# Performance work log

Hardware: AMD Instinct MI355X
Metric: run time of the kernel (lower is better)

Reference implementation:

```python
import jax, jax.numpy as jnp
import numpy as np

D_MODEL = 256
NUM_HEAD = 4
D_HEAD = D_MODEL // NUM_HEAD
B, N, M = 1, 512, 512


def setup_inputs() -> dict:
    key = jax.random.key(0)
    ks = jax.random.split(key, 13)
    s = 1.0 / np.sqrt(D_MODEL)
    inp = {
        'input_q': jax.random.normal(ks[0], (B, N, D_MODEL), jnp.float32),
        'input_k': jax.random.normal(ks[1], (B, M, D_MODEL), jnp.float32),
        'input_v': jax.random.normal(ks[2], (B, M, D_MODEL), jnp.float32),
        'input_p': jax.random.normal(ks[3], (B, N, M, D_MODEL), jnp.float32),
        'key_masks': jnp.zeros((B, M), dtype=bool),
        'Wq': jax.random.normal(ks[4], (D_MODEL, D_MODEL), jnp.float32) * s,
        'bq': jnp.zeros((D_MODEL,), jnp.float32),
        'Wk': jax.random.normal(ks[5], (D_MODEL, D_MODEL), jnp.float32) * s,
        'bk': jnp.zeros((D_MODEL,), jnp.float32),
        'Wv': jax.random.normal(ks[6], (D_MODEL, D_MODEL), jnp.float32) * s,
        'bv': jnp.zeros((D_MODEL,), jnp.float32),
        'Wp': jax.random.normal(ks[7], (D_MODEL, D_MODEL), jnp.float32) * s,
        'bp': jnp.zeros((D_MODEL,), jnp.float32),
    }
    return inp


def reference(input_q, input_k, input_v, input_p, key_masks,
              Wq, bq, Wk, bk, Wv, bv, Wp, bp):
    H, Dh = NUM_HEAD, D_HEAD
    b, n, _ = input_q.shape
    m = input_k.shape[1]
    # linear projections (PyTorch Linear: x @ W.T + b)
    q = (input_q @ Wq.T + bq).reshape(b, n, H, Dh).transpose(0, 2, 1, 3)   # (B,H,N,Dh)
    k = (input_k @ Wk.T + bk).reshape(b, m, H, Dh).transpose(0, 2, 1, 3)   # (B,H,M,Dh)
    v = (input_v @ Wv.T + bv).reshape(b, m, H, Dh).transpose(0, 2, 1, 3)   # (B,H,M,Dh)
    p = (input_p @ Wp.T + bp).reshape(b, n, m, H, Dh)                      # (B,N,M,H,Dh)
    # content scores + per-pair RPE scores (q dot p)
    scores = (jnp.einsum('bhnd,bhmd->bhnm', q, k)
              + jnp.einsum('bhnd,bnmhd->bhnm', q, p)) / np.sqrt(Dh)
    scores = jnp.where(key_masks[:, None, None, :], -jnp.inf, scores)
    attn = jax.nn.softmax(scores, axis=-1)                                 # (B,H,N,M)
    hidden = jnp.einsum('bhnm,bhmd->bhnd', attn, v)
    hidden = hidden.transpose(0, 2, 1, 3).reshape(b, n, H * Dh)            # (B,N,C)
    return hidden
```

## Files before the change

kernel.cpp:

```cpp
#include <hip/hip_runtime.h>
#include <math.h>

#define DMODEL 256
#define NSEQ   512
#define MSEQ   512
#define NHEAD  4
#define DHEAD  64

#define WS_Q      0
#define WS_K      131072
#define WS_V      262144
#define WS_WPE    393216
#define WS_SCORES 917504

__global__ __launch_bounds__(256) void proj_qkv(
    const float* __restrict__ xq, const float* __restrict__ xk,
    const float* __restrict__ xv,
    const float* __restrict__ Wq, const float* __restrict__ bq,
    const float* __restrict__ Wk, const float* __restrict__ bk,
    const float* __restrict__ Wv, const float* __restrict__ bv,
    float* __restrict__ ws)
{
    int bid = blockIdx.x;
    int mat = bid >> 6;
    int rb  = bid & 63;
    const float* X; const float* W; const float* b; float* Y;
    if (mat == 0)      { X = xq; W = Wq; b = bq; Y = ws + WS_Q; }
    else if (mat == 1) { X = xk; W = Wk; b = bk; Y = ws + WS_K; }
    else               { X = xv; W = Wv; b = bv; Y = ws + WS_V; }

    int c  = threadIdx.x;
    int r0 = rb * 8;
    float acc[8];
    float bias = b[c];
#pragma unroll
    for (int r = 0; r < 8; ++r) acc[r] = bias;

    const float4* Wrow = (const float4*)(W + (size_t)c * DMODEL);
    for (int d4 = 0; d4 < 64; ++d4) {
        float4 w = Wrow[d4];
#pragma unroll
        for (int r = 0; r < 8; ++r) {
            float4 x = ((const float4*)(X + (size_t)(r0 + r) * DMODEL))[d4];
            acc[r] += w.x * x.x + w.y * x.y + w.z * x.z + w.w * x.w;
        }
    }
#pragma unroll
    for (int r = 0; r < 8; ++r)
        Y[(size_t)(r0 + r) * DMODEL + c] = acc[r];
}

__global__ __launch_bounds__(256) void make_wpeff(
    const float* __restrict__ Wp, float* __restrict__ ws)
{
    const float* q   = ws + WS_Q;
    float*       wpe = ws + WS_WPE;
    int n0 = blockIdx.x * 2;
    int d  = threadIdx.x;

    const float* q0 = q + (size_t)n0 * DMODEL;
    const float* q1 = q0 + DMODEL;

    float acc0[4] = {0.f, 0.f, 0.f, 0.f};
    float acc1[4] = {0.f, 0.f, 0.f, 0.f};
#pragma unroll
    for (int h = 0; h < 4; ++h) {
        for (int dh = 0; dh < 64; ++dh) {
            int c = h * 64 + dh;
            float w = Wp[(size_t)c * DMODEL + d];
            acc0[h] += q0[c] * w;
            acc1[h] += q1[c] * w;
        }
    }
    *(float4*)&wpe[(size_t)n0 * 1024 + d * 4] =
        make_float4(acc0[0], acc0[1], acc0[2], acc0[3]);
    *(float4*)&wpe[(size_t)(n0 + 1) * 1024 + d * 4] =
        make_float4(acc1[0], acc1[1], acc1[2], acc1[3]);
}

__global__ __launch_bounds__(256) void p_scores(
    const float* __restrict__ Xp, float* __restrict__ ws)
{
    const float* wpe    = ws + WS_WPE;
    float*       scores = ws + WS_SCORES;

    int bid  = blockIdx.x;
    int n    = bid >> 1;
    int m0   = (bid & 1) * 256;
    int tid  = threadIdx.x;
    int wv   = tid >> 6;
    int lane = tid & 63;
    int p    = lane & 15;
    int r3   = lane >> 4;

    const float4* wp4 = (const float4*)(wpe + (size_t)n * 1024);
    float4 w[4][4];
#pragma unroll
    for (int j = 0; j < 4; ++j)
#pragma unroll
        for (int c = 0; c < 4; ++c)
            w[j][c] = wp4[4 * p + 64 * j + c];

    __shared__ float sm[4][256];

    const float4* base4 =
        (const float4*)Xp + ((size_t)n * MSEQ + m0 + wv * 64) * 64;

#pragma unroll 2
    for (int g = 0; g < 16; ++g) {
        int rbase = (g * 4 + r3) * 64 + p;
        float4 xv0 = base4[rbase + 0];
        float4 xv1 = base4[rbase + 16];
        float4 xv2 = base4[rbase + 32];
        float4 xv3 = base4[rbase + 48];

        float sh[4] = {0.f, 0.f, 0.f, 0.f};
        {
            const float4 xs[4] = {xv0, xv1, xv2, xv3};
#pragma unroll
            for (int j = 0; j < 4; ++j) {
                const float* xc = &xs[j].x;
#pragma unroll
                for (int c = 0; c < 4; ++c) {
                    const float* wf = &w[j][c].x;
#pragma unroll
                    for (int h = 0; h < 4; ++h)
                        sh[h] += xc[c] * wf[h];
                }
            }
        }
#pragma unroll
        for (int off = 1; off < 16; off <<= 1) {
#pragma unroll
            for (int h = 0; h < 4; ++h)
                sh[h] += __shfl_xor(sh[h], off);
        }
        if (p == 0) {
            int ml = wv * 64 + g * 4 + r3;
            sm[0][ml] = sh[0];
            sm[1][ml] = sh[1];
            sm[2][ml] = sh[2];
            sm[3][ml] = sh[3];
        }
    }
    __syncthreads();

    size_t ob = (size_t)n * MSEQ + m0 + tid;
    scores[0 * 262144 + ob] = sm[0][tid];
    scores[1 * 262144 + ob] = sm[1][tid];
    scores[2 * 262144 + ob] = sm[2][tid];
    scores[3 * 262144 + ob] = sm[3][tid];
}

__global__ __launch_bounds__(256) void qk_scores(
    const float* __restrict__ bp, float* __restrict__ ws)
{
    const float* q      = ws + WS_Q;
    const float* k      = ws + WS_K;
    float*       scores = ws + WS_SCORES;

    int bid = blockIdx.x;
    int h   = bid >> 6;
    int nt  = (bid >> 3) & 7;
    int mt  = bid & 7;
    int n0  = nt * 64, m0 = mt * 64;

    __shared__ float qs[64][76];
    __shared__ float ks[64][76];
    __shared__ float qb[64];

    int tid = threadIdx.x;
#pragma unroll
    for (int rep = 0; rep < 4; ++rep) {
        int idx = rep * 1024 + tid * 4;
        int row = idx >> 6, col = idx & 63;
        *(float4*)&qs[row][col] =
            *(const float4*)&q[(size_t)(n0 + row) * DMODEL + h * 64 + col];
        *(float4*)&ks[row][col] =
            *(const float4*)&k[(size_t)(m0 + row) * DMODEL + h * 64 + col];
    }
    __syncthreads();

    if (tid < 64) {
        float s = 0.f;
        for (int dh = 0; dh < 64; ++dh) s += qs[tid][dh] * bp[h * 64 + dh];
        qb[tid] = s;
    }
    __syncthreads();

    int tn = tid >> 4, tm = tid & 15;
    float acc[4][4] = {};
    for (int kk = 0; kk < 64; kk += 4) {
        float4 qf[4], kf[4];
#pragma unroll
        for (int i = 0; i < 4; ++i) {
            qf[i] = *(const float4*)&qs[tn * 4 + i][kk];
            kf[i] = *(const float4*)&ks[tm * 4 + i][kk];
        }
#pragma unroll
        for (int i = 0; i < 4; ++i)
#pragma unroll
            for (int j = 0; j < 4; ++j)
                acc[i][j] += qf[i].x * kf[j].x + qf[i].y * kf[j].y +
                             qf[i].z * kf[j].z + qf[i].w * kf[j].w;
    }

#pragma unroll
    for (int i = 0; i < 4; ++i) {
        int n = n0 + tn * 4 + i;
        float qbn = qb[tn * 4 + i];
        float4* pp = (float4*)&scores[(size_t)h * 262144 +
                                      (size_t)n * MSEQ + m0 + tm * 4];
        float4 sp = *pp;
        sp.x = 0.125f * (sp.x + acc[i][0] + qbn);
        sp.y = 0.125f * (sp.y + acc[i][1] + qbn);
        sp.z = 0.125f * (sp.z + acc[i][2] + qbn);
        sp.w = 0.125f * (sp.w + acc[i][3] + qbn);
        *pp = sp;
    }
}

__global__ __launch_bounds__(256) void softmax_av(
    const unsigned char* __restrict__ mask,
    float* __restrict__ out, float* __restrict__ ws)
{
    const float* v      = ws + WS_V;
    const float* scores = ws + WS_SCORES;

    int bid = blockIdx.x;
    int h   = bid >> 6;
    int g   = bid & 63;
    int n0  = g * 8;

    __shared__ float  pl[MSEQ * 9];
    __shared__ float4 red4[256];
    __shared__ float  wred[4];

    int tid  = threadIdx.x;
    int lane = tid & 63, wv = tid >> 6;

    for (int j = 0; j < 8; ++j) {
        int n = n0 + j;
        const float* srow = scores + (size_t)h * 262144 + (size_t)n * MSEQ;
        float s0 = srow[tid];
        float s1 = srow[tid + 256];
        if (mask[tid])       s0 = -INFINITY;
        if (mask[tid + 256]) s1 = -INFINITY;

        float mx = fmaxf(s0, s1);
#pragma unroll
        for (int off = 32; off; off >>= 1) mx = fmaxf(mx, __shfl_xor(mx, off));
        if (lane == 0) wred[wv] = mx;
        __syncthreads();
        mx = fmaxf(fmaxf(wred[0], wred[1]), fmaxf(wred[2], wred[3]));

        float e0 = __expf(s0 - mx);
        float e1 = __expf(s1 - mx);
        float sm = e0 + e1;
#pragma unroll
        for (int off = 32; off; off >>= 1) sm += __shfl_xor(sm, off);
        __syncthreads();
        if (lane == 0) wred[wv] = sm;
        __syncthreads();
        sm = wred[0] + wred[1] + wred[2] + wred[3];
        float rinv = 1.0f / sm;

        pl[(size_t)tid * 9 + j]         = e0 * rinv;
        pl[(size_t)(tid + 256) * 9 + j] = e1 * rinv;
        __syncthreads();
    }

    int dhq = tid & 15, mq = tid >> 4;
    float acc[8][4] = {};
    for (int i = 0; i < 32; ++i) {
        int m = i * 16 + mq;
        float4 vv = *(const float4*)&v[(size_t)m * DMODEL + h * 64 + dhq * 4];
        float4 pa = *(const float4*)&pl[(size_t)m * 9];
        float4 pb = *(const float4*)&pl[(size_t)m * 9 + 4];
#pragma unroll
        for (int j = 0; j < 4; ++j) {
            float pv = (&pa.x)[j];
            acc[j][0] += pv * vv.x; acc[j][1] += pv * vv.y;
            acc[j][2] += pv * vv.z; acc[j][3] += pv * vv.w;
        }
#pragma unroll
        for (int j = 0; j < 4; ++j) {
            float pv = (&pb.x)[j];
            acc[4 + j][0] += pv * vv.x; acc[4 + j][1] += pv * vv.y;
            acc[4 + j][2] += pv * vv.z; acc[4 + j][3] += pv * vv.w;
        }
    }

    for (int j = 0; j < 8; ++j) {
        red4[mq * 16 + dhq] =
            make_float4(acc[j][0], acc[j][1], acc[j][2], acc[j][3]);
        __syncthreads();
        if (tid < 64) {
            int dq = tid >> 2, x = tid & 3;
            float s = 0.f;
#pragma unroll
            for (int qq = 0; qq < 16; ++qq)
                s += ((const float*)&red4[qq * 16 + dq])[x];
            out[(size_t)(n0 + j) * DMODEL + h * 64 + tid] = s;
        }
        __syncthreads();
    }
}

extern "C" void kernel_launch(void* const* d_in, const int* in_sizes, int n_in,
                              void* d_out, int out_size, void* d_ws,
                              size_t ws_size, hipStream_t stream)
{
    const float* xq = (const float*)d_in[0];
    const float* xk = (const float*)d_in[1];
    const float* xv = (const float*)d_in[2];
    const float* xp = (const float*)d_in[3];
    const unsigned char* mask = (const unsigned char*)d_in[4];
    const float* Wq = (const float*)d_in[5];
    const float* bq = (const float*)d_in[6];
    const float* Wk = (const float*)d_in[7];
    const float* bk = (const float*)d_in[8];
    const float* Wv = (const float*)d_in[9];
    const float* bv = (const float*)d_in[10];
    const float* Wp = (const float*)d_in[11];
    const float* bp = (const float*)d_in[12];
    float* out = (float*)d_out;
    float* ws  = (float*)d_ws;

    proj_qkv  <<<192,  256, 0, stream>>>(xq, xk, xv, Wq, bq, Wk, bk, Wv, bv, ws);
    make_wpeff<<<256,  256, 0, stream>>>(Wp, ws);
    p_scores  <<<1024, 256, 0, stream>>>(xp, ws);
    qk_scores <<<256,  256, 0, stream>>>(bp, ws);
    softmax_av<<<256,  256, 0, stream>>>(mask, out, ws);
}
```

Before: 108.1 us.

## Reorder QK before P-scores, use nontemporal loads for P, restructure helper kernels

The QK score kernel now runs before the P-score kernel and writes scaled QK scores, and the P-score kernel accumulates its scaled contribution into them. This replaces the old read-modify-write pass in QK and restructures QK as a per-row-group dot product over keys. The large input_p stream is read with nontemporal loads to avoid polluting the cache. make_wpeff now uses one block per row with q staged in shared memory, and softmax_av's probability layout is changed from stride 9 to stride 8 with a contiguous m ordering. The risk is more LDS bank conflicts from the stride-8 layout, and the P kernel now does a read-add-write on the score buffer.

```diff
diff --git a/kernel.cpp b/kernel.cpp
--- a/kernel.cpp
+++ b/kernel.cpp
@@ -4,14 +4,14 @@
 #define DMODEL 256
 #define NSEQ   512
 #define MSEQ   512
-#define NHEAD  4
-#define DHEAD  64
 
 #define WS_Q      0
 #define WS_K      131072
 #define WS_V      262144
 #define WS_WPE    393216
-#define WS_SCORES 917504
+#define WS_SQK    917504
+
+typedef float v4f __attribute__((ext_vector_type(4)));
 
 __global__ __launch_bounds__(256) void proj_qkv(
     const float* __restrict__ xq, const float* __restrict__ xk,
@@ -55,34 +55,85 @@
 {
     const float* q   = ws + WS_Q;
     float*       wpe = ws + WS_WPE;
-    int n0 = blockIdx.x * 2;
-    int d  = threadIdx.x;
-
-    const float* q0 = q + (size_t)n0 * DMODEL;
-    const float* q1 = q0 + DMODEL;
-
-    float acc0[4] = {0.f, 0.f, 0.f, 0.f};
-    float acc1[4] = {0.f, 0.f, 0.f, 0.f};
+    int n = blockIdx.x;
+    int d = threadIdx.x;
+
+    __shared__ float ql[256];
+    ql[d] = q[(size_t)n * DMODEL + d];
+    __syncthreads();
+
+    float acc[4];
 #pragma unroll
     for (int h = 0; h < 4; ++h) {
+        float a = 0.f;
+#pragma unroll 8
         for (int dh = 0; dh < 64; ++dh) {
             int c = h * 64 + dh;
-            float w = Wp[(size_t)c * DMODEL + d];
-            acc0[h] += q0[c] * w;
-            acc1[h] += q1[c] * w;
-        }
-    }
-    *(float4*)&wpe[(size_t)n0 * 1024 + d * 4] =
-        make_float4(acc0[0], acc0[1], acc0[2], acc0[3]);
-    *(float4*)&wpe[(size_t)(n0 + 1) * 1024 + d * 4] =
-        make_float4(acc1[0], acc1[1], acc1[2], acc1[3]);
+            a += ql[c] * Wp[(size_t)c * DMODEL + d];
+        }
+        acc[h] = a;
+    }
+    *(float4*)&wpe[(size_t)n * 1024 + d * 4] =
+        make_float4(acc[0], acc[1], acc[2], acc[3]);
+}
+
+__global__ __launch_bounds__(256) void qk_scores(
+    const float* __restrict__ bp, float* __restrict__ ws)
+{
+    const float* q   = ws + WS_Q;
+    const float* k   = ws + WS_K;
+    float*       sqk = ws + WS_SQK;
+
+    int bid = blockIdx.x;
+    int h   = bid >> 6;
+    int g   = bid & 63;
+    int n0  = g * 8;
+    int tid = threadIdx.x;
+
+    __shared__ float qls[8][64];
+    __shared__ float qb[8];
+
+    if (tid < 128) {
+        int row = tid >> 4, col = (tid & 15) * 4;
+        *(float4*)&qls[row][col] =
+            *(const float4*)&q[(size_t)(n0 + row) * DMODEL + h * 64 + col];
+    }
+    __syncthreads();
+    if (tid < 8) {
+        float s = 0.f;
+        for (int dh = 0; dh < 64; ++dh) s += qls[tid][dh] * bp[h * 64 + dh];
+        qb[tid] = s;
+    }
+    __syncthreads();
+
+    const float* ka = k + (size_t)tid * DMODEL + h * 64;
+    const float* kb = ka + (size_t)256 * DMODEL;
+    float acca[8] = {};
+    float accb[8] = {};
+#pragma unroll 4
+    for (int d4 = 0; d4 < 16; ++d4) {
+        float4 xa = *(const float4*)(ka + d4 * 4);
+        float4 xb = *(const float4*)(kb + d4 * 4);
+#pragma unroll
+        for (int j = 0; j < 8; ++j) {
+            float4 qq = *(const float4*)&qls[j][d4 * 4];
+            acca[j] += xa.x * qq.x + xa.y * qq.y + xa.z * qq.z + xa.w * qq.w;
+            accb[j] += xb.x * qq.x + xb.y * qq.y + xb.z * qq.z + xb.w * qq.w;
+        }
+    }
+#pragma unroll
+    for (int j = 0; j < 8; ++j) {
+        size_t base = (size_t)h * 262144 + (size_t)(n0 + j) * MSEQ;
+        sqk[base + tid]       = 0.125f * (acca[j] + qb[j]);
+        sqk[base + tid + 256] = 0.125f * (accb[j] + qb[j]);
+    }
 }
 
 __global__ __launch_bounds__(256) void p_scores(
     const float* __restrict__ Xp, float* __restrict__ ws)
 {
-    const float* wpe    = ws + WS_WPE;
-    float*       scores = ws + WS_SCORES;
+    const float* wpe = ws + WS_WPE;
+    float*       sqk = ws + WS_SQK;
 
     int bid  = blockIdx.x;
     int n    = bid >> 1;
@@ -103,29 +154,29 @@
 
     __shared__ float sm[4][256];
 
-    const float4* base4 =
-        (const float4*)Xp + ((size_t)n * MSEQ + m0 + wv * 64) * 64;
+    const v4f* base4 =
+        (const v4f*)Xp + ((size_t)n * MSEQ + m0 + wv * 64) * 64;
 
 #pragma unroll 2
     for (int g = 0; g < 16; ++g) {
         int rbase = (g * 4 + r3) * 64 + p;
-        float4 xv0 = base4[rbase + 0];
-        float4 xv1 = base4[rbase + 16];
-        float4 xv2 = base4[rbase + 32];
-        float4 xv3 = base4[rbase + 48];
+        v4f xv0 = __builtin_nontemporal_load(&base4[rbase + 0]);
+        v4f xv1 = __builtin_nontemporal_load(&base4[rbase + 16]);
+        v4f xv2 = __builtin_nontemporal_load(&base4[rbase + 32]);
+        v4f xv3 = __builtin_nontemporal_load(&base4[rbase + 48]);
 
         float sh[4] = {0.f, 0.f, 0.f, 0.f};
         {
-            const float4 xs[4] = {xv0, xv1, xv2, xv3};
+            const v4f xs[4] = {xv0, xv1, xv2, xv3};
 #pragma unroll
             for (int j = 0; j < 4; ++j) {
-                const float* xc = &xs[j].x;
 #pragma unroll
                 for (int c = 0; c < 4; ++c) {
+                    const float xc = xs[j][c];
                     const float* wf = &w[j][c].x;
 #pragma unroll
                     for (int h = 0; h < 4; ++h)
-                        sh[h] += xc[c] * wf[h];
+                        sh[h] += xc * wf[h];
                 }
             }
         }
@@ -146,78 +197,9 @@
     __syncthreads();
 
     size_t ob = (size_t)n * MSEQ + m0 + tid;
-    scores[0 * 262144 + ob] = sm[0][tid];
-    scores[1 * 262144 + ob] = sm[1][tid];
-    scores[2 * 262144 + ob] = sm[2][tid];
-    scores[3 * 262144 + ob] = sm[3][tid];
-}
-
-__global__ __launch_bounds__(256) void qk_scores(
-    const float* __restrict__ bp, float* __restrict__ ws)
-{
-    const float* q      = ws + WS_Q;
-    const float* k      = ws + WS_K;
-    float*       scores = ws + WS_SCORES;
-
-    int bid = blockIdx.x;
-    int h   = bid >> 6;
-    int nt  = (bid >> 3) & 7;
-    int mt  = bid & 7;
-    int n0  = nt * 64, m0 = mt * 64;
-
-    __shared__ float qs[64][76];
-    __shared__ float ks[64][76];
-    __shared__ float qb[64];
-
-    int tid = threadIdx.x;
-#pragma unroll
-    for (int rep = 0; rep < 4; ++rep) {
-        int idx = rep * 1024 + tid * 4;
-        int row = idx >> 6, col = idx & 63;
-        *(float4*)&qs[row][col] =
-            *(const float4*)&q[(size_t)(n0 + row) * DMODEL + h * 64 + col];
-        *(float4*)&ks[row][col] =
-            *(const float4*)&k[(size_t)(m0 + row) * DMODEL + h * 64 + col];
-    }
-    __syncthreads();
-
-    if (tid < 64) {
-        float s = 0.f;
-        for (int dh = 0; dh < 64; ++dh) s += qs[tid][dh] * bp[h * 64 + dh];
-        qb[tid] = s;
-    }
-    __syncthreads();
-
-    int tn = tid >> 4, tm = tid & 15;
-    float acc[4][4] = {};
-    for (int kk = 0; kk < 64; kk += 4) {
-        float4 qf[4], kf[4];
-#pragma unroll
-        for (int i = 0; i < 4; ++i) {
-            qf[i] = *(const float4*)&qs[tn * 4 + i][kk];
-            kf[i] = *(const float4*)&ks[tm * 4 + i][kk];
-        }
-#pragma unroll
-        for (int i = 0; i < 4; ++i)
-#pragma unroll
-            for (int j = 0; j < 4; ++j)
-                acc[i][j] += qf[i].x * kf[j].x + qf[i].y * kf[j].y +
-                             qf[i].z * kf[j].z + qf[i].w * kf[j].w;
-    }
-
-#pragma unroll
-    for (int i = 0; i < 4; ++i) {
-        int n = n0 + tn * 4 + i;
-        float qbn = qb[tn * 4 + i];
-        float4* pp = (float4*)&scores[(size_t)h * 262144 +
-                                      (size_t)n * MSEQ + m0 + tm * 4];
-        float4 sp = *pp;
-        sp.x = 0.125f * (sp.x + acc[i][0] + qbn);
-        sp.y = 0.125f * (sp.y + acc[i][1] + qbn);
-        sp.z = 0.125f * (sp.z + acc[i][2] + qbn);
-        sp.w = 0.125f * (sp.w + acc[i][3] + qbn);
-        *pp = sp;
-    }
+#pragma unroll
+    for (int h = 0; h < 4; ++h)
+        sqk[h * 262144 + ob] += 0.125f * sm[h][tid];
 }
 
 __global__ __launch_bounds__(256) void softmax_av(
@@ -225,14 +207,14 @@
     float* __restrict__ out, float* __restrict__ ws)
 {
     const float* v      = ws + WS_V;
-    const float* scores = ws + WS_SCORES;
+    const float* scores = ws + WS_SQK;
 
     int bid = blockIdx.x;
     int h   = bid >> 6;
     int g   = bid & 63;
     int n0  = g * 8;
 
-    __shared__ float  pl[MSEQ * 9];
+    __shared__ float  pl[MSEQ * 8];
     __shared__ float4 red4[256];
     __shared__ float  wred[4];
 
@@ -265,18 +247,18 @@
         sm = wred[0] + wred[1] + wred[2] + wred[3];
         float rinv = 1.0f / sm;
 
-        pl[(size_t)tid * 9 + j]         = e0 * rinv;
-        pl[(size_t)(tid + 256) * 9 + j] = e1 * rinv;
+        pl[(size_t)tid * 8 + j]         = e0 * rinv;
+        pl[(size_t)(tid + 256) * 8 + j] = e1 * rinv;
         __syncthreads();
     }
 
     int dhq = tid & 15, mq = tid >> 4;
     float acc[8][4] = {};
     for (int i = 0; i < 32; ++i) {
-        int m = i * 16 + mq;
+        int m = mq * 32 + i;
         float4 vv = *(const float4*)&v[(size_t)m * DMODEL + h * 64 + dhq * 4];
-        float4 pa = *(const float4*)&pl[(size_t)m * 9];
-        float4 pb = *(const float4*)&pl[(size_t)m * 9 + 4];
+        float4 pa = *(const float4*)&pl[m * 8];
+        float4 pb = *(const float4*)&pl[m * 8 + 4];
 #pragma unroll
         for (int j = 0; j < 4; ++j) {
             float pv = (&pa.x)[j];
@@ -328,8 +310,8 @@
     float* ws  = (float*)d_ws;
 
     proj_qkv  <<<192,  256, 0, stream>>>(xq, xk, xv, Wq, bq, Wk, bk, Wv, bv, ws);
-    make_wpeff<<<256,  256, 0, stream>>>(Wp, ws);
+    make_wpeff<<<512,  256, 0, stream>>>(Wp, ws);
+    qk_scores <<<256,  256, 0, stream>>>(bp, ws);
     p_scores  <<<1024, 256, 0, stream>>>(xp, ws);
-    qk_scores <<<256,  256, 0, stream>>>(bp, ws);
     softmax_av<<<256,  256, 0, stream>>>(mask, out, ws);
 }
```

Measured after the change: 107.9 us. Within noise of the previous version (-0.2%).
